# Optimization experiments

Measured on AMD Instinct MI355X. Metric: run time of the kernel, lower is better.

The kernel has to match this reference:

```python
import jax, jax.numpy as jnp
import numpy as np

H = 128
B, N, E = 256, 81, 1620
LN_EPS = 1e-5


def setup_inputs() -> dict:
    key = jax.random.key(0)
    ks = jax.random.split(key, 12)
    s = 0.05
    return {
        "node_features": jax.random.normal(ks[0], (B, N, H), jnp.float32),
        "edge_index": jax.random.randint(ks[1], (2, E), 0, N, jnp.int64),
        "Wm1": jax.random.normal(ks[2], (2 * H, H), jnp.float32) * s,
        "bm1": jnp.zeros((H,), jnp.float32),
        "Wm2": jax.random.normal(ks[3], (H, H), jnp.float32) * s,
        "bm2": jnp.zeros((H,), jnp.float32),
        "Wu1": jax.random.normal(ks[4], (2 * H, H), jnp.float32) * s,
        "bu1": jnp.zeros((H,), jnp.float32),
        "Wu2": jax.random.normal(ks[5], (H, H), jnp.float32) * s,
        "bu2": jnp.zeros((H,), jnp.float32),
        "gamma": jnp.ones((H,), jnp.float32),
        "beta": jnp.zeros((H,), jnp.float32),
    }


def reference(node_features, edge_index, Wm1, bm1, Wm2, bm2, Wu1, bu1, Wu2, bu2, gamma, beta):
    src_idx, tgt_idx = edge_index[0], edge_index[1]
    # Gather: [B, E, H] each (vectorized over batch; original loops in Python)
    src = node_features[:, src_idx]
    tgt = node_features[:, tgt_idx]
    comb = jnp.concatenate([src, tgt], axis=-1)            # [B, E, 2H]
    msgs = jax.nn.relu(comb @ Wm1 + bm1) @ Wm2 + bm2       # [B, E, H]
    # Scatter-mean aggregation at target nodes
    agg = jnp.zeros_like(node_features).at[:, tgt_idx].add(msgs)  # [B, N, H]
    counts = jnp.zeros((N,), node_features.dtype).at[tgt_idx].add(1.0)
    counts = jnp.maximum(counts, 1.0)
    agg = agg / counts[None, :, None]
    # Node update MLP + residual + LayerNorm
    comb2 = jnp.concatenate([node_features, agg], axis=-1)  # [B, N, 2H]
    upd = jax.nn.relu(comb2 @ Wu1 + bu1) @ Wu2 + bu2
    x = node_features + upd
    mu = jnp.mean(x, axis=-1, keepdims=True)
    var = jnp.mean(jnp.square(x - mu), axis=-1, keepdims=True)
    return (x - mu) * jax.lax.rsqrt(var + LN_EPS) * gamma + beta
```

## Files before the change

kernel.cpp:

```cpp
#include <hip/hip_runtime.h>


#define NN 81
#define HH 128
#define EE 1620
#define NCH 12
#define CHSZ 135
#define MPAD 96
#define WB_BYTES 196608
#define OFFS_OFF (WB_BYTES)
#define CSR_OFF  (WB_BYTES + 82 * 4)
#define WS_NEED  (CSR_OFF + EE * 4)

typedef __attribute__((ext_vector_type(8))) short bf16x8;
typedef __attribute__((ext_vector_type(8))) unsigned short ushort8v;
typedef __attribute__((ext_vector_type(4))) unsigned short ushort4v;
typedef __attribute__((ext_vector_type(4))) float f32x4;

__device__ __forceinline__ unsigned short f2b(float f) {
  union { float f; unsigned u; } v; v.f = f;
  unsigned r = v.u + 0x7fffu + ((v.u >> 16) & 1u);
  return (unsigned short)(r >> 16);
}
__device__ __forceinline__ float b2f(unsigned short h) {
  union { unsigned u; float f; } v; v.u = ((unsigned)h) << 16;
  return v.f;
}

__global__ __launch_bounds__(1024)
void setup_kernel(const float* __restrict__ Wm1, const float* __restrict__ Wm2,
                  const float* __restrict__ Wu1, const float* __restrict__ Wu2,
                  const int* __restrict__ eidx, char* __restrict__ ws) {
  __shared__ int edg[2 * EE];
  __shared__ int cnt[NCH][NN];
  __shared__ int tot[NN];
  __shared__ int scanS[128];
  __shared__ int wsumS[2];
  __shared__ int offsS[NN + 1];
  __shared__ int csrS[EE];

  if (blockIdx.x < 12) {
    const int gid = blockIdx.x * 1024 + threadIdx.x;
    const int lane = gid & 63;
    const int t = gid >> 6;
    const int ks = t & 3, nt = (t >> 2) & 7, mat = t >> 5;
    const float* src;
    if (mat == 0) src = Wm1;
    else if (mat == 1) src = Wm1 + HH * HH;
    else if (mat == 2) src = Wm2;
    else if (mat == 3) src = Wu1;
    else if (mat == 4) src = Wu1 + HH * HH;
    else src = Wu2;
    const int c = nt * 16 + (lane & 15);
    const int k0 = ks * 32 + (lane >> 4) * 8;
    bf16x8 pv;
#pragma unroll
    for (int j = 0; j < 8; ++j) pv[j] = (short)f2b(src[(k0 + j) * HH + c]);
    *(bf16x8*)((unsigned short*)ws + (size_t)mat * 16384 + (((nt * 4 + ks) * 64) + lane) * 8) = pv;
    return;
  }

  const int tid = threadIdx.x;
  for (int i = tid; i < 2 * EE; i += 1024) edg[i] = eidx[i];
  __syncthreads();
  if (tid < NCH * NN) {
    const int t = tid % NN, ch = tid / NN;
    const int e0 = ch * CHSZ, e1 = e0 + CHSZ;
    int c = 0;
    for (int e = e0; e < e1; ++e) c += (edg[EE + e] == t);
    cnt[ch][tid / NN == ch ? t : t] = 0;
    cnt[ch][t] = c;
  }
  __syncthreads();
  if (tid < NN) {
    int s = 0;
#pragma unroll
    for (int ch = 0; ch < NCH; ++ch) s += cnt[ch][tid];
    tot[tid] = s;
  }
  __syncthreads();
  if (tid < 128) {
    const int l = tid & 63, w = tid >> 6;
    int inc = (tid < NN) ? tot[tid] : 0;
#pragma unroll
    for (int d = 1; d < 64; d <<= 1) {
      int u = __shfl_up(inc, d);
      if (l >= d) inc += u;
    }
    scanS[tid] = inc;
    if (l == 63) wsumS[w] = inc;
  }
  __syncthreads();
  if (tid < 128) {
    const int w = tid >> 6;
    const int inc = scanS[tid] + (w ? wsumS[0] : 0);
    if (tid < NN) offsS[tid] = inc - tot[tid];
    if (tid == NN - 1) offsS[NN] = inc;
  }
  __syncthreads();
  if (tid < NCH * NN) {
    const int t = tid % NN, ch = tid / NN;
    int pos = offsS[t];
    for (int c2 = 0; c2 < ch; ++c2) pos += cnt[c2][t];
    const int e0 = ch * CHSZ, e1 = e0 + CHSZ;
    for (int e = e0; e < e1; ++e)
      if (edg[EE + e] == t) csrS[pos++] = edg[e];
  }
  __syncthreads();
  int* wofs = (int*)(ws + OFFS_OFF);
  int* wcsr = (int*)(ws + CSR_OFF);
  for (int i = tid; i < NN + 1; i += 1024) wofs[i] = offsS[i];
  for (int i = tid; i < EE; i += 1024) wcsr[i] = csrS[i];
}

__device__ __forceinline__ void gemm3x1(const unsigned short* Ab, const unsigned short* Wp,
                                        int lane, int mt0, int nt0, f32x4 acc[3]) {
  bf16x8 Bf[4];
#pragma unroll
  for (int ks = 0; ks < 4; ++ks)
    Bf[ks] = *(const bf16x8*)(Wp + ((nt0 * 4 + ks) * 64 + lane) * 8);
  const int rl = lane & 15;
  const int kb = (lane >> 4) * 16;
  const unsigned swz = (unsigned)((rl & 7) << 4);
#pragma unroll
  for (int ks = 0; ks < 4; ++ks)
#pragma unroll
    for (int mm = 0; mm < 3; ++mm) {
      const int r = (mt0 + mm) * 16 + rl;
      const unsigned byte = (unsigned)(r * 256) + (((unsigned)(ks * 64 + kb)) ^ swz);
      bf16x8 a = *(const bf16x8*)((const char*)Ab + byte);
      acc[mm] = __builtin_amdgcn_mfma_f32_16x16x32_bf16(a, Bf[ks], acc[mm], 0, 0, 0);
    }
}

__device__ __forceinline__ void gemm3x1x2(const unsigned short* Ab,
                                          const unsigned short* Wp0, const unsigned short* Wp1,
                                          int lane, int mt0, int nt0,
                                          f32x4 acc0[3], f32x4 acc1[3]) {
  bf16x8 B0[4], B1[4];
#pragma unroll
  for (int ks = 0; ks < 4; ++ks) {
    B0[ks] = *(const bf16x8*)(Wp0 + ((nt0 * 4 + ks) * 64 + lane) * 8);
    B1[ks] = *(const bf16x8*)(Wp1 + ((nt0 * 4 + ks) * 64 + lane) * 8);
  }
  const int rl = lane & 15;
  const int kb = (lane >> 4) * 16;
  const unsigned swz = (unsigned)((rl & 7) << 4);
#pragma unroll
  for (int ks = 0; ks < 4; ++ks)
#pragma unroll
    for (int mm = 0; mm < 3; ++mm) {
      const int r = (mt0 + mm) * 16 + rl;
      const unsigned byte = (unsigned)(r * 256) + (((unsigned)(ks * 64 + kb)) ^ swz);
      bf16x8 a = *(const bf16x8*)((const char*)Ab + byte);
      acc0[mm] = __builtin_amdgcn_mfma_f32_16x16x32_bf16(a, B0[ks], acc0[mm], 0, 0, 0);
      acc1[mm] = __builtin_amdgcn_mfma_f32_16x16x32_bf16(a, B1[ks], acc1[mm], 0, 0, 0);
    }
}

__global__ __launch_bounds__(1024, 4)
void mpnn_mfma2_kernel(const float* __restrict__ node,
                       const float* __restrict__ bm1, const float* __restrict__ bm2,
                       const float* __restrict__ bu1, const float* __restrict__ bu2,
                       const float* __restrict__ gamma_, const float* __restrict__ beta_,
                       const char* __restrict__ ws,
                       float* __restrict__ out) {
  __shared__ float X[NN][HH];
  __shared__ unsigned short Xb[MPAD * HH];
  __shared__ unsigned short bufP[MPAD * HH];
  __shared__ unsigned short bufQ[MPAD * HH];
  __shared__ int   csrL[EE];
  __shared__ int   offsL[NN + 1];
  __shared__ float bias[6][HH];

  const int tid  = threadIdx.x;
  const int lane = tid & 63;
  const int wave = tid >> 6;
  const int b    = blockIdx.x;

  const unsigned short* wpk = (const unsigned short*)ws;
  const int* wofs = (const int*)(ws + OFFS_OFF);
  const int* wcsr = (const int*)(ws + CSR_OFF);

  {
    const float4* nf4 = (const float4*)(node + (size_t)b * NN * HH);
    for (int i = tid; i < NN * HH / 4; i += 1024) {
      float4 v = nf4[i];
      const int f = i * 4, r = f >> 7, c = f & 127;
      *(float4*)&X[r][c] = v;
      ushort4v pv = { f2b(v.x), f2b(v.y), f2b(v.z), f2b(v.w) };
      const unsigned byte = ((unsigned)(r * 256 + c * 2)) ^ ((unsigned)((r & 7) << 4));
      *(ushort4v*)((char*)Xb + byte) = pv;
    }
    if (tid < (MPAD - NN) * 16) {
      const int r = NN + tid / 16, m = tid % 16;
      const unsigned byte = ((unsigned)(r * 256 + m * 16)) ^ ((unsigned)((r & 7) << 4));
      ushort8v z = {0,0,0,0,0,0,0,0};
      *(ushort8v*)((char*)Xb + byte) = z;
    }
    for (int i = tid; i < EE; i += 1024) csrL[i] = wcsr[i];
    if (tid < NN + 1) offsL[tid] = wofs[tid];
    if (tid < HH) {
      bias[0][tid] = bm1[tid]; bias[1][tid] = bm2[tid];
      bias[2][tid] = bu1[tid]; bias[3][tid] = bu2[tid];
      bias[4][tid] = gamma_[tid]; bias[5][tid] = beta_[tid];
    }
  }
  __syncthreads();

  const int nt0 = wave & 7;
  const int mt0 = 3 * (wave >> 3);
  const int erow = (lane >> 4) * 4;
  const int ecol = lane & 15;

  f32x4 accU[3];
  {
    f32x4 accP[3], accQ[3];
#pragma unroll
    for (int mm = 0; mm < 3; ++mm) { accP[mm] = (f32x4)0.f; accQ[mm] = (f32x4)0.f; accU[mm] = (f32x4)0.f; }
    gemm3x1x2(Xb, wpk, wpk + 16384, lane, mt0, nt0, accP, accQ);
    gemm3x1(Xb, wpk + 3 * 16384, lane, mt0, nt0, accU);
#pragma unroll
    for (int mm = 0; mm < 3; ++mm)
#pragma unroll
      for (int rg = 0; rg < 4; ++rg) {
        const int R = (mt0 + mm) * 16 + erow + rg;
        const int C = nt0 * 16 + ecol;
        const unsigned byte = ((unsigned)(R * 256 + C * 2)) ^ ((unsigned)((R & 7) << 4));
        const bool ok = (R < NN);
        *(unsigned short*)((char*)bufP + byte) = ok ? f2b(accP[mm][rg]) : (unsigned short)0;
        *(unsigned short*)((char*)bufQ + byte) = ok ? f2b(accQ[mm][rg]) : (unsigned short)0;
      }
  }
  __syncthreads();

  {
    const float bm1a = bias[0][2 * lane];
    const float bm1b = bias[0][2 * lane + 1];
    for (int t = wave; t < NN; t += 16) {
      const unsigned qbyte = ((unsigned)(t * 256 + lane * 4)) ^ ((unsigned)((t & 7) << 4));
      const unsigned pq = *(const unsigned*)((const char*)bufQ + qbyte);
      const float q0 = b2f((unsigned short)(pq & 0xffff)) + bm1a;
      const float q1 = b2f((unsigned short)(pq >> 16))    + bm1b;
      float h0 = 0.f, h1 = 0.f;
      const int o0 = offsL[t], o1 = offsL[t + 1];
      for (int e = o0; e < o1; ++e) {
        const int s = csrL[e];
        const unsigned pb = ((unsigned)(s * 256 + lane * 4)) ^ ((unsigned)((s & 7) << 4));
        const unsigned pp = *(const unsigned*)((const char*)bufP + pb);
        h0 += fmaxf(b2f((unsigned short)(pp & 0xffff)) + q0, 0.f);
        h1 += fmaxf(b2f((unsigned short)(pp >> 16))    + q1, 0.f);
      }
      const unsigned hv = (unsigned)f2b(h0) | ((unsigned)f2b(h1) << 16);
      *(unsigned*)((char*)bufQ + qbyte) = hv;
    }
  }
  __syncthreads();

  {
    f32x4 acc[3];
#pragma unroll
    for (int mm = 0; mm < 3; ++mm) acc[mm] = (f32x4)0.f;
    gemm3x1(bufQ, wpk + 2 * 16384, lane, mt0, nt0, acc);
#pragma unroll
    for (int mm = 0; mm < 3; ++mm)
#pragma unroll
      for (int rg = 0; rg < 4; ++rg) {
        const int R = (mt0 + mm) * 16 + erow + rg;
        const int C = nt0 * 16 + ecol;
        float v = 0.f;
        if (R < NN) {
          const float dg = (float)(offsL[R + 1] - offsL[R]);
          v = (acc[mm][rg] + dg * bias[1][C]) * (1.f / fmaxf(dg, 1.f));
        }
        const unsigned byte = ((unsigned)(R * 256 + C * 2)) ^ ((unsigned)((R & 7) << 4));
        *(unsigned short*)((char*)bufP + byte) = f2b(v);
      }
  }
  __syncthreads();

  {
    gemm3x1(bufP, wpk + 4 * 16384, lane, mt0, nt0, accU);
#pragma unroll
    for (int mm = 0; mm < 3; ++mm)
#pragma unroll
      for (int rg = 0; rg < 4; ++rg) {
        const int R = (mt0 + mm) * 16 + erow + rg;
        const int C = nt0 * 16 + ecol;
        const float v = (R < NN) ? fmaxf(accU[mm][rg] + bias[2][C], 0.f) : 0.f;
        const unsigned byte = ((unsigned)(R * 256 + C * 2)) ^ ((unsigned)((R & 7) << 4));
        *(unsigned short*)((char*)bufQ + byte) = f2b(v);
      }
  }
  __syncthreads();

  {
    f32x4 acc[3];
#pragma unroll
    for (int mm = 0; mm < 3; ++mm) acc[mm] = (f32x4)0.f;
    gemm3x1(bufQ, wpk + 5 * 16384, lane, mt0, nt0, acc);
#pragma unroll
    for (int mm = 0; mm < 3; ++mm)
#pragma unroll
      for (int rg = 0; rg < 4; ++rg) {
        const int R = (mt0 + mm) * 16 + erow + rg;
        const int C = nt0 * 16 + ecol;
        if (R < NN) X[R][C] += acc[mm][rg] + bias[3][C];
      }
  }
  __syncthreads();

  for (int r = wave; r < NN; r += 16) {
    const float x0 = X[r][lane], x1 = X[r][lane + 64];
    float s = x0 + x1;
#pragma unroll
    for (int off = 32; off; off >>= 1) s += __shfl_xor(s, off);
    const float mu = s * (1.f / 128.f);
    const float d0 = x0 - mu, d1 = x1 - mu;
    float v = d0 * d0 + d1 * d1;
#pragma unroll
    for (int off = 32; off; off >>= 1) v += __shfl_xor(v, off);
    const float rstd = rsqrtf(v * (1.f / 128.f) + 1e-5f);
    const size_t o = ((size_t)b * NN + r) * HH;
    out[o + lane]      = d0 * rstd * bias[4][lane]      + bias[5][lane];
    out[o + lane + 64] = d1 * rstd * bias[4][lane + 64] + bias[5][lane + 64];
  }
}

__device__ __forceinline__ void gemm_acc_f32(const float (*A)[HH], const float* __restrict__ Wg,
                                             int c, int row0, int nr, float (&acc)[41]) {
  float w[8];
#pragma unroll
  for (int j = 0; j < 8; ++j) w[j] = Wg[j * HH + c];
  for (int k0 = 0; k0 < HH; k0 += 8) {
    float wn[8];
    if (k0 + 8 < HH) {
#pragma unroll
      for (int j = 0; j < 8; ++j) wn[j] = Wg[(k0 + 8 + j) * HH + c];
    }
#pragma unroll
    for (int i = 0; i < 41; ++i) {
      if (i < nr) {
        const float4 a0 = *(const float4*)&A[row0 + i][k0];
        const float4 a1 = *(const float4*)&A[row0 + i][k0 + 4];
        acc[i] += a0.x * w[0] + a0.y * w[1] + a0.z * w[2] + a0.w * w[3]
                + a1.x * w[4] + a1.y * w[5] + a1.z * w[6] + a1.w * w[7];
      }
    }
#pragma unroll
    for (int j = 0; j < 8; ++j) w[j] = wn[j];
  }
}

__global__ __launch_bounds__(256, 1)
void mpnn_fused_kernel(const float* __restrict__ node, const int* __restrict__ eidx,
                       const float* __restrict__ Wm1, const float* __restrict__ bm1,
                       const float* __restrict__ Wm2, const float* __restrict__ bm2,
                       const float* __restrict__ Wu1, const float* __restrict__ bu1,
                       const float* __restrict__ Wu2, const float* __restrict__ bu2,
                       const float* __restrict__ gamma_, const float* __restrict__ beta_,
                       float* __restrict__ out) {
  __shared__ float X[NN][HH];
  __shared__ float Pb[NN][HH];
  __shared__ float Qb[NN][HH];
  __shared__ int   edg[2 * EE];
  __shared__ int   csr[EE];
  __shared__ int   offs[NN + 1];
  __shared__ int   cnt3[3][NN];
  __shared__ int   base3[3][NN];
  __shared__ float biases[6][HH];

  const int tid  = threadIdx.x;
  const int lane = tid & 63;
  const int wave = tid >> 6;
  const int b    = blockIdx.x;

  {
    const float4* nf4 = (const float4*)(node + (size_t)b * NN * HH);
    float4* X4 = (float4*)&X[0][0];
    for (int i = tid; i < NN * HH / 4; i += 256) X4[i] = nf4[i];
    for (int i = tid; i < 2 * EE; i += 256) edg[i] = eidx[i];
    if (tid < HH) {
      biases[0][tid] = bm1[tid]; biases[1][tid] = bm2[tid];
      biases[2][tid] = bu1[tid]; biases[3][tid] = bu2[tid];
      biases[4][tid] = gamma_[tid]; biases[5][tid] = beta_[tid];
    }
  }
  __syncthreads();
  if (tid < 3 * NN) {
    const int t = tid % NN, ch = tid / NN;
    const int e0 = ch * 540, e1 = e0 + 540;
    int cnt = 0;
    for (int e = e0; e < e1; ++e) cnt += (edg[EE + e] == t);
    cnt3[ch][t] = cnt;
  }
  __syncthreads();
  if (tid == 0) {
    int run = 0;
    for (int t = 0; t < NN; ++t) {
      offs[t] = run;
      base3[0][t] = run;
      base3[1][t] = base3[0][t] + cnt3[0][t];
      base3[2][t] = base3[1][t] + cnt3[1][t];
      run = base3[2][t] + cnt3[2][t];
    }
    offs[NN] = run;
  }
  __syncthreads();
  if (tid < 3 * NN) {
    const int t = tid % NN, ch = tid / NN;
    const int e0 = ch * 540, e1 = e0 + 540;
    int pos = base3[ch][t];
    for (int e = e0; e < e1; ++e)
      if (edg[EE + e] == t) csr[pos++] = edg[e];
  }
  __syncthreads();

  const int c    = ((wave & 1) << 6) | lane;
  const int row0 = (wave >> 1) ? 41 : 0;
  const int nr   = (wave >> 1) ? 40 : 41;

  {
    float acc[41];
#pragma unroll
    for (int i = 0; i < 41; ++i) acc[i] = 0.f;
    gemm_acc_f32(X, Wm1, c, row0, nr, acc);
#pragma unroll
    for (int i = 0; i < 41; ++i) if (i < nr) Pb[row0 + i][c] = acc[i];
  }
  {
    float acc[41];
#pragma unroll
    for (int i = 0; i < 41; ++i) acc[i] = 0.f;
    gemm_acc_f32(X, Wm1 + HH * HH, c, row0, nr, acc);
#pragma unroll
    for (int i = 0; i < 41; ++i) if (i < nr) Qb[row0 + i][c] = acc[i];
  }
  __syncthreads();

  for (int t = wave; t < NN; t += 4) {
    const int o0 = offs[t], o1 = offs[t + 1];
    const float q0 = Qb[t][lane]      + biases[0][lane];
    const float q1 = Qb[t][lane + 64] + biases[0][lane + 64];
    float h0 = 0.f, h1 = 0.f;
    for (int e = o0; e < o1; ++e) {
      const int s = csr[e];
      h0 += fmaxf(Pb[s][lane]      + q0, 0.f);
      h1 += fmaxf(Pb[s][lane + 64] + q1, 0.f);
    }
    Qb[t][lane]      = h0;
    Qb[t][lane + 64] = h1;
  }
  __syncthreads();

  {
    float acc[41];
#pragma unroll
    for (int i = 0; i < 41; ++i) acc[i] = 0.f;
    gemm_acc_f32(Qb, Wm2, c, row0, nr, acc);
#pragma unroll
    for (int i = 0; i < 41; ++i) if (i < nr) {
      const int r = row0 + i;
      const float d = (float)(offs[r + 1] - offs[r]);
      Pb[r][c] = (acc[i] + d * biases[1][c]) * (1.f / fmaxf(d, 1.f));
    }
  }
  __syncthreads();

  {
    float acc[41];
#pragma unroll
    for (int i = 0; i < 41; ++i) acc[i] = 0.f;
    gemm_acc_f32(X,  Wu1,           c, row0, nr, acc);
    gemm_acc_f32(Pb, Wu1 + HH * HH, c, row0, nr, acc);
#pragma unroll
    for (int i = 0; i < 41; ++i) if (i < nr)
      Qb[row0 + i][c] = fmaxf(acc[i] + biases[2][c], 0.f);
  }
  __syncthreads();

  {
    float acc[41];
#pragma unroll
    for (int i = 0; i < 41; ++i) acc[i] = 0.f;
    gemm_acc_f32(Qb, Wu2, c, row0, nr, acc);
#pragma unroll
    for (int i = 0; i < 41; ++i) if (i < nr) {
      const int r = row0 + i;
      X[r][c] = X[r][c] + acc[i] + biases[3][c];
    }
  }
  __syncthreads();

  for (int r = wave; r < NN; r += 4) {
    const float x0 = X[r][lane], x1 = X[r][lane + 64];
    float s = x0 + x1;
#pragma unroll
    for (int off = 32; off; off >>= 1) s += __shfl_xor(s, off);
    const float mu = s * (1.f / 128.f);
    const float d0 = x0 - mu, d1 = x1 - mu;
    float v = d0 * d0 + d1 * d1;
#pragma unroll
    for (int off = 32; off; off >>= 1) v += __shfl_xor(v, off);
    const float rstd = rsqrtf(v * (1.f / 128.f) + 1e-5f);
    const size_t o = ((size_t)b * NN + r) * HH;
    out[o + lane]      = d0 * rstd * biases[4][lane]      + biases[5][lane];
    out[o + lane + 64] = d1 * rstd * biases[4][lane + 64] + biases[5][lane + 64];
  }
}

extern "C" void kernel_launch(void* const* d_in, const int* in_sizes, int n_in,
                              void* d_out, int out_size, void* d_ws, size_t ws_size,
                              hipStream_t stream) {
  (void)in_sizes; (void)n_in; (void)out_size;
  const float* node  = (const float*)d_in[0];
  const int*   eidx  = (const int*)  d_in[1];
  const float* Wm1   = (const float*)d_in[2];
  const float* bm1   = (const float*)d_in[3];
  const float* Wm2   = (const float*)d_in[4];
  const float* bm2   = (const float*)d_in[5];
  const float* Wu1   = (const float*)d_in[6];
  const float* bu1   = (const float*)d_in[7];
  const float* Wu2   = (const float*)d_in[8];
  const float* bu2   = (const float*)d_in[9];
  const float* gamma_= (const float*)d_in[10];
  const float* beta_ = (const float*)d_in[11];
  float* outp = (float*)d_out;

  if (ws_size >= (size_t)WS_NEED) {
    char* ws = (char*)d_ws;
    hipLaunchKernelGGL(setup_kernel, dim3(13), dim3(1024), 0, stream,
                       Wm1, Wm2, Wu1, Wu2, eidx, ws);
    hipLaunchKernelGGL(mpnn_mfma2_kernel, dim3(256), dim3(1024), 0, stream,
                       node, bm1, bm2, bu1, bu2, gamma_, beta_, ws, outp);
  } else {
    hipLaunchKernelGGL(mpnn_fused_kernel, dim3(256), dim3(256), 0, stream,
                       node, eidx, Wm1, bm1, Wm2, bm2, Wu1, bu1, Wu2, bu2,
                       gamma_, beta_, outp);
  }
}
```

Measured before the change: 46.96 us.

## Fold Wm2 into Wu1 bottom half to drop a GEMM stage and barrier

Because the scatter-mean is linear, the setup kernel precomputes Wm2·Wu1[H:] (plus bm2·Wu1[H:] as a combined bias) and packs the product as a bf16 MFMA operand. The main kernel then runs one dual-A GEMM (aggregated hidden × fused weight, node × Wu1 top) followed by the update ReLU, which removes one full GEMM pass, an LDS round trip and a __syncthreads. The edge-gather loop is also unrolled by four with split accumulators. In exchange the setup kernel does an fp32 128×128×128 matmul on four extra blocks, and rounding the fused weight to bf16 changes numerics slightly.

```diff
diff --git a/kernel.cpp b/kernel.cpp
--- a/kernel.cpp
+++ b/kernel.cpp
@@ -9,8 +9,9 @@
 #define MPAD 96
 #define WB_BYTES 196608
 #define OFFS_OFF (WB_BYTES)
-#define CSR_OFF  (WB_BYTES + 82 * 4)
-#define WS_NEED  (CSR_OFF + EE * 4)
+#define CSR_OFF  (OFFS_OFF + 82 * 4)
+#define BC_OFF   (CSR_OFF + EE * 4)
+#define WS_NEED  (BC_OFF + HH * 4)
 
 typedef __attribute__((ext_vector_type(8))) short bf16x8;
 typedef __attribute__((ext_vector_type(8))) unsigned short ushort8v;
@@ -26,91 +27,133 @@
   union { unsigned u; float f; } v; v.u = ((unsigned)h) << 16;
   return v.f;
 }
+__device__ __forceinline__ unsigned swzu(int r, int laneb) {
+  return ((unsigned)(r * 256 + laneb)) ^ ((unsigned)((r & 7) << 4));
+}
 
 __global__ __launch_bounds__(1024)
 void setup_kernel(const float* __restrict__ Wm1, const float* __restrict__ Wm2,
                   const float* __restrict__ Wu1, const float* __restrict__ Wu2,
-                  const int* __restrict__ eidx, char* __restrict__ ws) {
-  __shared__ int edg[2 * EE];
-  __shared__ int cnt[NCH][NN];
-  __shared__ int tot[NN];
-  __shared__ int scanS[128];
-  __shared__ int wsumS[2];
-  __shared__ int offsS[NN + 1];
-  __shared__ int csrS[EE];
-
-  if (blockIdx.x < 12) {
-    const int gid = blockIdx.x * 1024 + threadIdx.x;
+                  const float* __restrict__ bm2, const int* __restrict__ eidx,
+                  char* __restrict__ ws) {
+  __shared__ __align__(16) char arena[81920];
+  const int tid = threadIdx.x;
+
+  if (blockIdx.x < 8) {
+    const int gid = blockIdx.x * 1024 + tid;
     const int lane = gid & 63;
     const int t = gid >> 6;
     const int ks = t & 3, nt = (t >> 2) & 7, mat = t >> 5;
     const float* src;
-    if (mat == 0) src = Wm1;
-    else if (mat == 1) src = Wm1 + HH * HH;
-    else if (mat == 2) src = Wm2;
-    else if (mat == 3) src = Wu1;
-    else if (mat == 4) src = Wu1 + HH * HH;
-    else src = Wu2;
+    int slot;
+    if (mat == 0)      { src = Wm1;           slot = 0; }
+    else if (mat == 1) { src = Wm1 + HH * HH; slot = 1; }
+    else if (mat == 2) { src = Wu1;           slot = 3; }
+    else               { src = Wu2;           slot = 5; }
     const int c = nt * 16 + (lane & 15);
     const int k0 = ks * 32 + (lane >> 4) * 8;
     bf16x8 pv;
 #pragma unroll
     for (int j = 0; j < 8; ++j) pv[j] = (short)f2b(src[(k0 + j) * HH + c]);
-    *(bf16x8*)((unsigned short*)ws + (size_t)mat * 16384 + (((nt * 4 + ks) * 64) + lane) * 8) = pv;
+    *(bf16x8*)((unsigned short*)ws + (size_t)slot * 16384 + (((nt * 4 + ks) * 64) + lane) * 8) = pv;
     return;
   }
 
-  const int tid = threadIdx.x;
-  for (int i = tid; i < 2 * EE; i += 1024) edg[i] = eidx[i];
-  __syncthreads();
-  if (tid < NCH * NN) {
-    const int t = tid % NN, ch = tid / NN;
-    const int e0 = ch * CHSZ, e1 = e0 + CHSZ;
-    int c = 0;
-    for (int e = e0; e < e1; ++e) c += (edg[EE + e] == t);
-    cnt[ch][tid / NN == ch ? t : t] = 0;
-    cnt[ch][t] = c;
-  }
-  __syncthreads();
-  if (tid < NN) {
-    int s = 0;
-#pragma unroll
-    for (int ch = 0; ch < NCH; ++ch) s += cnt[ch][tid];
-    tot[tid] = s;
-  }
-  __syncthreads();
-  if (tid < 128) {
-    const int l = tid & 63, w = tid >> 6;
-    int inc = (tid < NN) ? tot[tid] : 0;
-#pragma unroll
-    for (int d = 1; d < 64; d <<= 1) {
-      int u = __shfl_up(inc, d);
-      if (l >= d) inc += u;
-    }
-    scanS[tid] = inc;
-    if (l == 63) wsumS[w] = inc;
-  }
-  __syncthreads();
-  if (tid < 128) {
-    const int w = tid >> 6;
-    const int inc = scanS[tid] + (w ? wsumS[0] : 0);
-    if (tid < NN) offsS[tid] = inc - tot[tid];
-    if (tid == NN - 1) offsS[NN] = inc;
-  }
-  __syncthreads();
-  if (tid < NCH * NN) {
-    const int t = tid % NN, ch = tid / NN;
-    int pos = offsS[t];
-    for (int c2 = 0; c2 < ch; ++c2) pos += cnt[c2][t];
-    const int e0 = ch * CHSZ, e1 = e0 + CHSZ;
-    for (int e = e0; e < e1; ++e)
-      if (edg[EE + e] == t) csrS[pos++] = edg[e];
-  }
-  __syncthreads();
-  int* wofs = (int*)(ws + OFFS_OFF);
-  int* wcsr = (int*)(ws + CSR_OFF);
-  for (int i = tid; i < NN + 1; i += 1024) wofs[i] = offsS[i];
-  for (int i = tid; i < EE; i += 1024) wcsr[i] = csrS[i];
+  if (blockIdx.x == 8) {
+    int* edg   = (int*)arena;
+    int* cnt   = edg + 2 * EE;
+    int* tot   = cnt + NCH * NN;
+    int* scanS = tot + NN;
+    int* wsumS = scanS + 128;
+    int* offsS = wsumS + 2;
+    int* csrS  = offsS + NN + 1;
+    for (int i = tid; i < 2 * EE; i += 1024) edg[i] = eidx[i];
+    __syncthreads();
+    if (tid < NCH * NN) {
+      const int t = tid % NN, ch = tid / NN;
+      const int e0 = ch * CHSZ, e1 = e0 + CHSZ;
+      int c = 0;
+      for (int e = e0; e < e1; ++e) c += (edg[EE + e] == t);
+      cnt[ch * NN + t] = c;
+    }
+    __syncthreads();
+    if (tid < NN) {
+      int s = 0;
+#pragma unroll
+      for (int ch = 0; ch < NCH; ++ch) s += cnt[ch * NN + tid];
+      tot[tid] = s;
+    }
+    __syncthreads();
+    if (tid < 128) {
+      const int l = tid & 63, w = tid >> 6;
+      int inc = (tid < NN) ? tot[tid] : 0;
+#pragma unroll
+      for (int d = 1; d < 64; d <<= 1) {
+        int u = __shfl_up(inc, d);
+        if (l >= d) inc += u;
+      }
+      scanS[tid] = inc;
+      if (l == 63) wsumS[w] = inc;
+    }
+    __syncthreads();
+    if (tid < 128) {
+      const int w = tid >> 6;
+      const int inc = scanS[tid] + (w ? wsumS[0] : 0);
+      if (tid < NN) offsS[tid] = inc - tot[tid];
+      if (tid == NN - 1) offsS[NN] = inc;
+    }
+    __syncthreads();
+    if (tid < NCH * NN) {
+      const int t = tid % NN, ch = tid / NN;
+      int pos = offsS[t];
+      for (int c2 = 0; c2 < ch; ++c2) pos += cnt[c2 * NN + t];
+      const int e0 = ch * CHSZ, e1 = e0 + CHSZ;
+      for (int e = e0; e < e1; ++e)
+        if (edg[EE + e] == t) csrS[pos++] = edg[e];
+    }
+    __syncthreads();
+    int* wofs = (int*)(ws + OFFS_OFF);
+    int* wcsr = (int*)(ws + CSR_OFF);
+    for (int i = tid; i < NN + 1; i += 1024) wofs[i] = offsS[i];
+    for (int i = tid; i < EE; i += 1024) wcsr[i] = csrS[i];
+    return;
+  }
+
+  {
+    const int bs = blockIdx.x - 9;
+    float* WuL = (float*)arena;
+    float* WmL = WuL + HH * HH;
+    const float* Wu1b = Wu1 + HH * HH;
+    float4* WuL4 = (float4*)WuL;
+    const float4* src4 = (const float4*)Wu1b;
+    for (int i = tid; i < HH * HH / 4; i += 1024) WuL4[i] = src4[i];
+    const float4* wm4 = (const float4*)(Wm2 + bs * 32 * HH);
+    float4* WmL4 = (float4*)WmL;
+    if (tid < 32 * HH / 4) WmL4[tid] = wm4[tid];
+    __syncthreads();
+    const int kk = tid >> 5;
+    const int k  = bs * 32 + kk;
+    const int cg = tid & 31;
+    f32x4 acc = (f32x4)0.f;
+    for (int j = 0; j < HH; ++j) {
+      const float a = WmL[kk * HH + j];
+      const float4 w = WuL4[j * 32 + cg];
+      acc[0] += a * w.x; acc[1] += a * w.y; acc[2] += a * w.z; acc[3] += a * w.w;
+    }
+    unsigned short* dst = (unsigned short*)ws;
+#pragma unroll
+    for (int q = 0; q < 4; ++q) {
+      const int c = cg * 4 + q;
+      const int nt = c >> 4;
+      const int l = (((k & 31) >> 3) << 4) | (c & 15);
+      dst[(size_t)2 * 16384 + (((nt * 4 + bs) * 64) + l) * 8 + (k & 7)] = f2b(acc[q]);
+    }
+    if (bs == 0 && tid < HH) {
+      float s = 0.f;
+      for (int j = 0; j < HH; ++j) s += bm2[j] * WuL[j * HH + tid];
+      ((float*)(ws + BC_OFF))[tid] = s;
+    }
+  }
 }
 
 __device__ __forceinline__ void gemm3x1(const unsigned short* Ab, const unsigned short* Wp,
@@ -158,9 +201,35 @@
     }
 }
 
+__device__ __forceinline__ void gemm3x1_2A(const unsigned short* A0, const unsigned short* A1,
+                                           const unsigned short* Wp0, const unsigned short* Wp1,
+                                           int lane, int mt0, int nt0,
+                                           f32x4 acc0[3], f32x4 acc1[3]) {
+  bf16x8 B0[4], B1[4];
+#pragma unroll
+  for (int ks = 0; ks < 4; ++ks) {
+    B0[ks] = *(const bf16x8*)(Wp0 + ((nt0 * 4 + ks) * 64 + lane) * 8);
+    B1[ks] = *(const bf16x8*)(Wp1 + ((nt0 * 4 + ks) * 64 + lane) * 8);
+  }
+  const int rl = lane & 15;
+  const int kb = (lane >> 4) * 16;
+  const unsigned swz = (unsigned)((rl & 7) << 4);
+#pragma unroll
+  for (int ks = 0; ks < 4; ++ks)
+#pragma unroll
+    for (int mm = 0; mm < 3; ++mm) {
+      const int r = (mt0 + mm) * 16 + rl;
+      const unsigned byte = (unsigned)(r * 256) + (((unsigned)(ks * 64 + kb)) ^ swz);
+      bf16x8 a0 = *(const bf16x8*)((const char*)A0 + byte);
+      acc0[mm] = __builtin_amdgcn_mfma_f32_16x16x32_bf16(a0, B0[ks], acc0[mm], 0, 0, 0);
+      bf16x8 a1 = *(const bf16x8*)((const char*)A1 + byte);
+      acc1[mm] = __builtin_amdgcn_mfma_f32_16x16x32_bf16(a1, B1[ks], acc1[mm], 0, 0, 0);
+    }
+}
+
 __global__ __launch_bounds__(1024, 4)
-void mpnn_mfma2_kernel(const float* __restrict__ node,
-                       const float* __restrict__ bm1, const float* __restrict__ bm2,
+void mpnn_mfma3_kernel(const float* __restrict__ node,
+                       const float* __restrict__ bm1,
                        const float* __restrict__ bu1, const float* __restrict__ bu2,
                        const float* __restrict__ gamma_, const float* __restrict__ beta_,
                        const char* __restrict__ ws,
@@ -181,6 +250,7 @@
   const unsigned short* wpk = (const unsigned short*)ws;
   const int* wofs = (const int*)(ws + OFFS_OFF);
   const int* wcsr = (const int*)(ws + CSR_OFF);
+  const float* wbc = (const float*)(ws + BC_OFF);
 
   {
     const float4* nf4 = (const float4*)(node + (size_t)b * NN * HH);
@@ -189,20 +259,18 @@
       const int f = i * 4, r = f >> 7, c = f & 127;
       *(float4*)&X[r][c] = v;
       ushort4v pv = { f2b(v.x), f2b(v.y), f2b(v.z), f2b(v.w) };
-      const unsigned byte = ((unsigned)(r * 256 + c * 2)) ^ ((unsigned)((r & 7) << 4));
-      *(ushort4v*)((char*)Xb + byte) = pv;
+      *(ushort4v*)((char*)Xb + swzu(r, c * 2)) = pv;
     }
     if (tid < (MPAD - NN) * 16) {
       const int r = NN + tid / 16, m = tid % 16;
-      const unsigned byte = ((unsigned)(r * 256 + m * 16)) ^ ((unsigned)((r & 7) << 4));
       ushort8v z = {0,0,0,0,0,0,0,0};
-      *(ushort8v*)((char*)Xb + byte) = z;
+      *(ushort8v*)((char*)Xb + swzu(r, m * 16)) = z;
     }
     for (int i = tid; i < EE; i += 1024) csrL[i] = wcsr[i];
     if (tid < NN + 1) offsL[tid] = wofs[tid];
     if (tid < HH) {
-      bias[0][tid] = bm1[tid]; bias[1][tid] = bm2[tid];
-      bias[2][tid] = bu1[tid]; bias[3][tid] = bu2[tid];
+      bias[0][tid] = bm1[tid];  bias[1][tid] = wbc[tid];
+      bias[2][tid] = bu1[tid];  bias[3][tid] = bu2[tid];
       bias[4][tid] = gamma_[tid]; bias[5][tid] = beta_[tid];
     }
   }
@@ -213,20 +281,18 @@
   const int erow = (lane >> 4) * 4;
   const int ecol = lane & 15;
 
-  f32x4 accU[3];
   {
     f32x4 accP[3], accQ[3];
 #pragma unroll
-    for (int mm = 0; mm < 3; ++mm) { accP[mm] = (f32x4)0.f; accQ[mm] = (f32x4)0.f; accU[mm] = (f32x4)0.f; }
+    for (int mm = 0; mm < 3; ++mm) { accP[mm] = (f32x4)0.f; accQ[mm] = (f32x4)0.f; }
     gemm3x1x2(Xb, wpk, wpk + 16384, lane, mt0, nt0, accP, accQ);
-    gemm3x1(Xb, wpk + 3 * 16384, lane, mt0, nt0, accU);
 #pragma unroll
     for (int mm = 0; mm < 3; ++mm)
 #pragma unroll
       for (int rg = 0; rg < 4; ++rg) {
         const int R = (mt0 + mm) * 16 + erow + rg;
         const int C = nt0 * 16 + ecol;
-        const unsigned byte = ((unsigned)(R * 256 + C * 2)) ^ ((unsigned)((R & 7) << 4));
+        const unsigned byte = swzu(R, C * 2);
         const bool ok = (R < NN);
         *(unsigned short*)((char*)bufP + byte) = ok ? f2b(accP[mm][rg]) : (unsigned short)0;
         *(unsigned short*)((char*)bufQ + byte) = ok ? f2b(accQ[mm][rg]) : (unsigned short)0;
@@ -237,20 +303,37 @@
   {
     const float bm1a = bias[0][2 * lane];
     const float bm1b = bias[0][2 * lane + 1];
+    const int lb = lane * 4;
     for (int t = wave; t < NN; t += 16) {
-      const unsigned qbyte = ((unsigned)(t * 256 + lane * 4)) ^ ((unsigned)((t & 7) << 4));
+      const unsigned qbyte = swzu(t, lb);
       const unsigned pq = *(const unsigned*)((const char*)bufQ + qbyte);
       const float q0 = b2f((unsigned short)(pq & 0xffff)) + bm1a;
       const float q1 = b2f((unsigned short)(pq >> 16))    + bm1b;
-      float h0 = 0.f, h1 = 0.f;
-      const int o0 = offsL[t], o1 = offsL[t + 1];
-      for (int e = o0; e < o1; ++e) {
+      float h0 = 0.f, h1 = 0.f, g0 = 0.f, g1 = 0.f;
+      int e = offsL[t];
+      const int o1 = offsL[t + 1];
+      for (; e + 4 <= o1; e += 4) {
+        const int s0 = csrL[e], s1 = csrL[e + 1], s2 = csrL[e + 2], s3 = csrL[e + 3];
+        const unsigned p0 = *(const unsigned*)((const char*)bufP + swzu(s0, lb));
+        const unsigned p1 = *(const unsigned*)((const char*)bufP + swzu(s1, lb));
+        const unsigned p2 = *(const unsigned*)((const char*)bufP + swzu(s2, lb));
+        const unsigned p3 = *(const unsigned*)((const char*)bufP + swzu(s3, lb));
+        h0 += fmaxf(b2f((unsigned short)(p0 & 0xffff)) + q0, 0.f);
+        h1 += fmaxf(b2f((unsigned short)(p0 >> 16))    + q1, 0.f);
+        g0 += fmaxf(b2f((unsigned short)(p1 & 0xffff)) + q0, 0.f);
+        g1 += fmaxf(b2f((unsigned short)(p1 >> 16))    + q1, 0.f);
+        h0 += fmaxf(b2f((unsigned short)(p2 & 0xffff)) + q0, 0.f);
+        h1 += fmaxf(b2f((unsigned short)(p2 >> 16))    + q1, 0.f);
+        g0 += fmaxf(b2f((unsigned short)(p3 & 0xffff)) + q0, 0.f);
+        g1 += fmaxf(b2f((unsigned short)(p3 >> 16))    + q1, 0.f);
+      }
+      for (; e < o1; ++e) {
         const int s = csrL[e];
-        const unsigned pb = ((unsigned)(s * 256 + lane * 4)) ^ ((unsigned)((s & 7) << 4));
-        const unsigned pp = *(const unsigned*)((const char*)bufP + pb);
+        const unsigned pp = *(const unsigned*)((const char*)bufP + swzu(s, lb));
         h0 += fmaxf(b2f((unsigned short)(pp & 0xffff)) + q0, 0.f);
         h1 += fmaxf(b2f((unsigned short)(pp >> 16))    + q1, 0.f);
       }
+      h0 += g0; h1 += g1;
       const unsigned hv = (unsigned)f2b(h0) | ((unsigned)f2b(h1) << 16);
       *(unsigned*)((char*)bufQ + qbyte) = hv;
     }
@@ -258,10 +341,10 @@
   __syncthreads();
 
   {
-    f32x4 acc[3];
-#pragma unroll
-    for (int mm = 0; mm < 3; ++mm) acc[mm] = (f32x4)0.f;
-    gemm3x1(bufQ, wpk + 2 * 16384, lane, mt0, nt0, acc);
+    f32x4 accT[3], accU[3];
+#pragma unroll
+    for (int mm = 0; mm < 3; ++mm) { accT[mm] = (f32x4)0.f; accU[mm] = (f32x4)0.f; }
+    gemm3x1_2A(bufQ, Xb, wpk + 2 * 16384, wpk + 3 * 16384, lane, mt0, nt0, accT, accU);
 #pragma unroll
     for (int mm = 0; mm < 3; ++mm)
 #pragma unroll
@@ -270,35 +353,21 @@
         const int C = nt0 * 16 + ecol;
         float v = 0.f;
         if (R < NN) {
-          const float dg = (float)(offsL[R + 1] - offsL[R]);
-          v = (acc[mm][rg] + dg * bias[1][C]) * (1.f / fmaxf(dg, 1.f));
+          const int dg = offsL[R + 1] - offsL[R];
+          const float inv = (dg > 0) ? 1.f / (float)dg : 1.f;
+          const float sf  = (dg > 0) ? 1.f : 0.f;
+          v = fmaxf(accU[mm][rg] + accT[mm][rg] * inv + sf * bias[1][C] + bias[2][C], 0.f);
         }
-        const unsigned byte = ((unsigned)(R * 256 + C * 2)) ^ ((unsigned)((R & 7) << 4));
-        *(unsigned short*)((char*)bufP + byte) = f2b(v);
+        *(unsigned short*)((char*)bufP + swzu(R, C * 2)) = f2b(v);
       }
   }
   __syncthreads();
 
   {
-    gemm3x1(bufP, wpk + 4 * 16384, lane, mt0, nt0, accU);
-#pragma unroll
-    for (int mm = 0; mm < 3; ++mm)
-#pragma unroll
-      for (int rg = 0; rg < 4; ++rg) {
-        const int R = (mt0 + mm) * 16 + erow + rg;
-        const int C = nt0 * 16 + ecol;
-        const float v = (R < NN) ? fmaxf(accU[mm][rg] + bias[2][C], 0.f) : 0.f;
-        const unsigned byte = ((unsigned)(R * 256 + C * 2)) ^ ((unsigned)((R & 7) << 4));
-        *(unsigned short*)((char*)bufQ + byte) = f2b(v);
-      }
-  }
-  __syncthreads();
-
-  {
     f32x4 acc[3];
 #pragma unroll
     for (int mm = 0; mm < 3; ++mm) acc[mm] = (f32x4)0.f;
-    gemm3x1(bufQ, wpk + 5 * 16384, lane, mt0, nt0, acc);
+    gemm3x1(bufP, wpk + 5 * 16384, lane, mt0, nt0, acc);
 #pragma unroll
     for (int mm = 0; mm < 3; ++mm)
 #pragma unroll
@@ -530,9 +599,9 @@
   if (ws_size >= (size_t)WS_NEED) {
     char* ws = (char*)d_ws;
     hipLaunchKernelGGL(setup_kernel, dim3(13), dim3(1024), 0, stream,
-                       Wm1, Wm2, Wu1, Wu2, eidx, ws);
-    hipLaunchKernelGGL(mpnn_mfma2_kernel, dim3(256), dim3(1024), 0, stream,
-                       node, bm1, bm2, bu1, bu2, gamma_, beta_, ws, outp);
+                       Wm1, Wm2, Wu1, Wu2, bm2, eidx, ws);
+    hipLaunchKernelGGL(mpnn_mfma3_kernel, dim3(256), dim3(1024), 0, stream,
+                       node, bm1, bu1, bu2, gamma_, beta_, ws, outp);
   } else {
     hipLaunchKernelGGL(mpnn_fused_kernel, dim3(256), dim3(256), 0, stream,
                        node, eidx, Wm1, bm1, Wm2, bm2, Wu1, bu1, Wu2, bu2,
```

New measurement: 45.50 us. 3.1% less time.
